# Kernel optimization log

Measured on AMD Instinct MI355X. Metric: run time of the kernel, lower is better.

## Reference

```python
import jax, jax.numpy as jnp
import numpy as np

D = 1024
H = 16
HD = D // H
EPS = 1e-5
NEG = -1e20


def _layernorm(x, w, b):
    m = jnp.mean(x, axis=-1, keepdims=True)
    v = jnp.mean((x - m) ** 2, axis=-1, keepdims=True)
    return (x - m) * jax.lax.rsqrt(v + EPS) * w + b


def setup_inputs() -> dict:
    key = jax.random.key(0)
    ks = jax.random.split(key, 16)
    s = 0.02
    inp = {
        "X": jax.random.normal(ks[0], (2, 2048, D), jnp.float32),
        "Wq": jax.random.normal(ks[1], (D, D), jnp.float32) * s,
        "bq": jnp.zeros((D,), jnp.float32),
        "Wk": jax.random.normal(ks[2], (D, D), jnp.float32) * s,
        "bk": jnp.zeros((D,), jnp.float32),
        "Wv": jax.random.normal(ks[3], (D, D), jnp.float32) * s,
        "bv": jnp.zeros((D,), jnp.float32),
        "Wo": jax.random.normal(ks[4], (D, D), jnp.float32) * s,
        "bo": jnp.zeros((D,), jnp.float32),
        "ln1_w": jnp.ones((D,), jnp.float32),
        "ln1_b": jnp.zeros((D,), jnp.float32),
        "Wup": jax.random.normal(ks[5], (4 * D, D), jnp.float32) * s,
        "bup": jnp.zeros((4 * D,), jnp.float32),
        "Wdown": jax.random.normal(ks[6], (D, 4 * D), jnp.float32) * s,
        "bdown": jnp.zeros((D,), jnp.float32),
        "ln2_w": jnp.ones((D,), jnp.float32),
        "ln2_b": jnp.zeros((D,), jnp.float32),
    }
    return inp


def reference(X, Wq, bq, Wk, bk, Wv, bv, Wo, bo, ln1_w, ln1_b,
              Wup, bup, Wdown, bdown, ln2_w, ln2_b):
    B, S, _ = X.shape
    # QKV projections -> [B, H, S, HD]
    q = (X @ Wq.T + bq).reshape(B, S, H, HD).transpose(0, 2, 1, 3)
    k = (X @ Wk.T + bk).reshape(B, S, H, HD).transpose(0, 2, 1, 3)
    v = (X @ Wv.T + bv).reshape(B, S, H, HD).transpose(0, 2, 1, 3)
    scores = jnp.einsum("bhqd,bhkd->bhqk", q, k) / jnp.sqrt(jnp.float32(HD))
    causal = jnp.tril(jnp.ones((S, S), dtype=bool))  # mask==0 -> -1e20
    scores = jnp.where(causal, scores, jnp.float32(NEG))
    attn = jax.nn.softmax(scores, axis=-1)  # dropout is identity in eval
    out = jnp.einsum("bhqk,bhkd->bhqd", attn, v)
    out = out.transpose(0, 2, 1, 3).reshape(B, S, D)
    out = out @ Wo.T + bo
    x = _layernorm(X + out, ln1_w, ln1_b)  # post-LN attention block
    up = jax.nn.relu(x @ Wup.T + bup)
    down = up @ Wdown.T + bdown
    return _layernorm(x + down, ln2_w, ln2_b)
```

## Files before the change

### kernel.cpp

```cpp
#include <hip/hip_runtime.h>
#include <stdint.h>

#define DMODEL 1024
#define NHEAD 16
#define HDIM 64
#define SEQ 2048
#define NBATCH 2
#define MTOK 4096

typedef float f32x4 __attribute__((ext_vector_type(4)));
typedef short s16x8 __attribute__((ext_vector_type(8)));
typedef unsigned short u16;
typedef u16 u16x4 __attribute__((ext_vector_type(4)));

typedef __attribute__((address_space(1))) const void* as1_cvp;
typedef __attribute__((address_space(3))) void* as3_vp;

__device__ inline u16 f2bf(float f) {
  uint32_t u = __float_as_uint(f);
  u = u + 0x7FFFu + ((u >> 16) & 1u);
  return (u16)(u >> 16);
}

__device__ inline uint32_t pk_bf16(float lo, float hi) {
  uint32_t r;
  asm("v_cvt_pk_bf16_f32 %0, %1, %2" : "=v"(r) : "v"(lo), "v"(hi));
  return r;
}

__device__ inline void gload_lds16(const void* g, void* l) {
  __builtin_amdgcn_global_load_lds((as1_cvp)g, (as3_vp)l, 16, 0, 0);
}

__global__ __launch_bounds__(256) void k_f2bf(const float* __restrict__ src,
                                              u16* __restrict__ dst, int n4) {
  int i = blockIdx.x * 256 + threadIdx.x;
  int stride = gridDim.x * 256;
  for (; i < n4; i += stride) {
    f32x4 v = ((const f32x4*)src)[i];
    u16x4 o;
    o[0] = f2bf(v[0]); o[1] = f2bf(v[1]); o[2] = f2bf(v[2]); o[3] = f2bf(v[3]);
    ((u16x4*)dst)[i] = o;
  }
}

__global__ __launch_bounds__(256) void k_f2bf_w4(
    const float* __restrict__ s0, const float* __restrict__ s1,
    const float* __restrict__ s2, const float* __restrict__ s3,
    u16* __restrict__ d0, u16* __restrict__ d1, u16* __restrict__ d2,
    u16* __restrict__ d3, int n4) {
  const float* src = blockIdx.y == 0 ? s0 : blockIdx.y == 1 ? s1
                     : blockIdx.y == 2 ? s2 : s3;
  u16* dst = blockIdx.y == 0 ? d0 : blockIdx.y == 1 ? d1
             : blockIdx.y == 2 ? d2 : d3;
  int i = blockIdx.x * 256 + threadIdx.x;
  int stride = gridDim.x * 256;
  for (; i < n4; i += stride) {
    f32x4 v = ((const f32x4*)src)[i];
    u16x4 o;
    o[0] = f2bf(v[0]); o[1] = f2bf(v[1]); o[2] = f2bf(v[2]); o[3] = f2bf(v[3]);
    ((u16x4*)dst)[i] = o;
  }
}

template <int MODE, int KSPL, int MH>
__global__ __launch_bounds__(512, 2) void k_gemm256(
    const u16* __restrict__ A, const u16* __restrict__ B,
    const float* __restrict__ bias, void* __restrict__ Cv,
    void* __restrict__ Cv1, int M, int N, int K) {
  constexpr int HALVES = MH + 2;
  __shared__ alignas(16) u16 lds[2 * HALVES * 8192];
  const int t = threadIdx.x;
  const int w = t >> 6;
  const int l = t & 63;
  const int wr = w >> 2;
  const int wc = w & 3;
  const int lr = l & 15, lg = l >> 4;
  const int r7 = lr & 7;
  const int lrow8 = l >> 3;

  const int gx = gridDim.x;
  int lin = blockIdx.y * gx + blockIdx.x;
  const int nwg = gx * gridDim.y;
  lin = (lin & 7) * (nwg >> 3) + (lin >> 3);
  const int bx = lin % gx, by = lin / gx;
  const int kz = KSPL > 1 ? blockIdx.z : 0;
  const int Kc = K / KSPL, kbeg = kz * Kc;
  const int brow = by * (MH * 128), bcol = bx * 256;

  constexpr int MF = MH * 4;
  const f32x4 Z4 = {0.f, 0.f, 0.f, 0.f};
  f32x4 acc[MF][4];
#pragma unroll
  for (int m = 0; m < MF; m++)
#pragma unroll
    for (int n = 0; n < 4; n++) acc[m][n] = Z4;

  const u16* Ag = A + (size_t)brow * K + kbeg;
  const u16* Bg = B + (size_t)bcol * K + kbeg;
  const int swz_src = ((l & 7) ^ ((l >> 3) & 7)) << 3;

  auto ldsH = [&](int buf, int half) { return lds + (buf * HALVES + half) * 8192; };
  auto stageA = [&](int kt, int buf) {
#pragma unroll
    for (int h = 0; h < MH; h++) {
      u16* lb = ldsH(buf, h);
      const int rb = h * 128;
      gload_lds16(Ag + (size_t)(rb + w * 8 + lrow8) * K + kt * 64 + swz_src,
                  lb + w * 512);
      gload_lds16(Ag + (size_t)(rb + 64 + w * 8 + lrow8) * K + kt * 64 + swz_src,
                  lb + (8 + w) * 512);
    }
  };
  auto stageB = [&](int kt, int buf) {
#pragma unroll
    for (int h = 0; h < 2; h++) {
      u16* lb = ldsH(buf, MH + h);
      const int rb = h * 128;
      gload_lds16(Bg + (size_t)(rb + w * 8 + lrow8) * K + kt * 64 + swz_src,
                  lb + w * 512);
      gload_lds16(Bg + (size_t)(rb + 64 + w * 8 + lrow8) * K + kt * 64 + swz_src,
                  lb + (8 + w) * 512);
    }
  };

  stageA(0, 0);
  stageB(0, 0);

  const int nkt = Kc >> 6;
  const int arb = (MH == 2) ? 0 : wr * 64;
  const int brb = (wc & 1) * 64;
  for (int kt = 0; kt < nkt; ++kt) {
    const int cur = kt & 1, nx = cur ^ 1;
    if (kt + 1 < nkt) {
      stageA(kt + 1, nx);
      if (MH == 2)
        asm volatile("s_waitcnt vmcnt(4)" ::: "memory");
      else
        asm volatile("s_waitcnt vmcnt(2)" ::: "memory");
    } else {
      asm volatile("s_waitcnt vmcnt(0)" ::: "memory");
    }
    __builtin_amdgcn_s_barrier();
    __builtin_amdgcn_sched_barrier(0);
    const u16* Ah = ldsH(cur, (MH == 2) ? wr : 0);
    const u16* Bh = ldsH(cur, MH + (wc >> 1));
#pragma unroll
    for (int kk = 0; kk < 2; kk++) {
      s16x8 bfr[4];
#pragma unroll
      for (int nf = 0; nf < 4; nf++)
        bfr[nf] = *(const s16x8*)(Bh + (brb + nf * 16 + lr) * 64 +
                                  (((kk * 4 + lg) ^ r7) << 3));
#pragma unroll
      for (int mh = 0; mh < MH; mh++) {
        s16x8 afr[4];
#pragma unroll
        for (int i = 0; i < 4; i++)
          afr[i] = *(const s16x8*)(Ah + (arb + (mh * 4 + i) * 16 + lr) * 64 +
                                   (((kk * 4 + lg) ^ r7) << 3));
        __builtin_amdgcn_s_setprio(1);
#pragma unroll
        for (int i = 0; i < 4; i++)
#pragma unroll
          for (int nf = 0; nf < 4; nf++)
            acc[mh * 4 + i][nf] = __builtin_amdgcn_mfma_f32_16x16x32_bf16(
                afr[i], bfr[nf], acc[mh * 4 + i][nf], 0, 0, 0);
        __builtin_amdgcn_s_setprio(0);
      }
      if (kk == 0 && kt + 1 < nkt) stageB(kt + 1, nx);
    }
    __builtin_amdgcn_sched_barrier(0);
    __builtin_amdgcn_s_barrier();
  }

  const int lg4 = lg * 4;
  const int wrb = wr * (MH == 2 ? 128 : 64);
  if (MODE == 0) {
    float* Co = (kz == 0) ? (float*)Cv : (float*)Cv1;
#pragma unroll
    for (int nf = 0; nf < 4; nf++) {
      const int col = bcol + wc * 64 + nf * 16 + lr;
      const float bvv = (kz == 0) ? bias[col] : 0.0f;
#pragma unroll
      for (int mf = 0; mf < MF; mf++) {
        const int row0 = brow + wrb + mf * 16 + lg4;
#pragma unroll
        for (int r = 0; r < 4; r++)
          Co[(size_t)(row0 + r) * N + col] = acc[mf][nf][r] + bvv;
      }
    }
  } else {
    u16* Sgw = lds + w * 2176;
    float bn[4];
#pragma unroll
    for (int nf = 0; nf < 4; nf++) bn[nf] = bias[bcol + wc * 64 + nf * 16 + lr];
    const int ch = l & 7;
#pragma unroll
    for (int hh = 0; hh < MH * 2; hh++) {
#pragma unroll
      for (int mm = 0; mm < 2; mm++) {
        const int mf = hh * 2 + mm;
#pragma unroll
        for (int nf = 0; nf < 4; nf++)
#pragma unroll
          for (int r = 0; r < 4; r++) {
            float vv = acc[mf][nf][r] + bn[nf];
            if (MODE == 2) vv = vv > 0.f ? vv : 0.f;
            Sgw[(mm * 16 + lg4 + r) * 68 + nf * 16 + lr] = f2bf(vv);
          }
      }
#pragma unroll
      for (int i = 0; i < 4; i++) {
        const int rr = i * 8 + (l >> 3);
        u16x4 a0 = *(const u16x4*)(Sgw + rr * 68 + ch * 8);
        u16x4 a1 = *(const u16x4*)(Sgw + rr * 68 + ch * 8 + 4);
        s16x8 v8;
#pragma unroll
        for (int j = 0; j < 4; j++) { v8[j] = (short)a0[j]; v8[4 + j] = (short)a1[j]; }
        *(s16x8*)((u16*)Cv + (size_t)(brow + wrb + hh * 32 + rr) * N +
                  (bcol + wc * 64 + ch * 8)) = v8;
      }
    }
  }
}

__global__ __launch_bounds__(512, 2) void k_gemm256_qkv(
    const u16* __restrict__ A, const u16* __restrict__ B,
    const float* __restrict__ bq, const float* __restrict__ bk,
    const float* __restrict__ bv, u16* __restrict__ qbf, u16* __restrict__ kbf,
    u16* __restrict__ vtbf, int M, int N, int K) {
  __shared__ alignas(16) u16 lds[2 * 4 * 8192];
  const int t = threadIdx.x;
  const int w = t >> 6, l = t & 63;
  const int wr = w >> 2, wc = w & 3;
  const int lr = l & 15, lg = l >> 4;
  const int r7 = lr & 7;
  const int lrow8 = l >> 3;

  const int gx = gridDim.x;
  int lin = blockIdx.y * gx + blockIdx.x;
  const int nwg = gx * gridDim.y;
  lin = (lin & 7) * (nwg >> 3) + (lin >> 3);
  const int bx = lin % gx, by = lin / gx;
  const int brow = by * 256, bcol = bx * 256;

  const f32x4 Z4 = {0.f, 0.f, 0.f, 0.f};
  f32x4 acc[8][4];
#pragma unroll
  for (int m = 0; m < 8; m++)
#pragma unroll
    for (int n = 0; n < 4; n++) acc[m][n] = Z4;

  const u16* Ag = A + (size_t)brow * K;
  const u16* Bg = B + (size_t)bcol * K;
  const int swz_src = ((l & 7) ^ ((l >> 3) & 7)) << 3;

  auto ldsH = [&](int buf, int half) { return lds + (buf * 4 + half) * 8192; };
  auto stageA = [&](int kt, int buf) {
#pragma unroll
    for (int h = 0; h < 2; h++) {
      u16* lb = ldsH(buf, h);
      const int rb = h * 128;
      gload_lds16(Ag + (size_t)(rb + w * 8 + lrow8) * K + kt * 64 + swz_src,
                  lb + w * 512);
      gload_lds16(Ag + (size_t)(rb + 64 + w * 8 + lrow8) * K + kt * 64 + swz_src,
                  lb + (8 + w) * 512);
    }
  };
  auto stageB = [&](int kt, int buf) {
#pragma unroll
    for (int h = 0; h < 2; h++) {
      u16* lb = ldsH(buf, 2 + h);
      const int rb = h * 128;
      gload_lds16(Bg + (size_t)(rb + w * 8 + lrow8) * K + kt * 64 + swz_src,
                  lb + w * 512);
      gload_lds16(Bg + (size_t)(rb + 64 + w * 8 + lrow8) * K + kt * 64 + swz_src,
                  lb + (8 + w) * 512);
    }
  };

  stageA(0, 0);
  stageB(0, 0);

  const int nkt = K >> 6;
  const int brb = (wc & 1) * 64;
  for (int kt = 0; kt < nkt; ++kt) {
    const int cur = kt & 1, nx = cur ^ 1;
    if (kt + 1 < nkt) {
      stageA(kt + 1, nx);
      asm volatile("s_waitcnt vmcnt(4)" ::: "memory");
    } else {
      asm volatile("s_waitcnt vmcnt(0)" ::: "memory");
    }
    __builtin_amdgcn_s_barrier();
    __builtin_amdgcn_sched_barrier(0);
    const u16* Ah = ldsH(cur, wr);
    const u16* Bh = ldsH(cur, 2 + (wc >> 1));
#pragma unroll
    for (int kk = 0; kk < 2; kk++) {
      s16x8 bfr[4];
#pragma unroll
      for (int nf = 0; nf < 4; nf++)
        bfr[nf] = *(const s16x8*)(Bh + (brb + nf * 16 + lr) * 64 +
                                  (((kk * 4 + lg) ^ r7) << 3));
#pragma unroll
      for (int mh = 0; mh < 2; mh++) {
        s16x8 afr[4];
#pragma unroll
        for (int i = 0; i < 4; i++)
          afr[i] = *(const s16x8*)(Ah + ((mh * 4 + i) * 16 + lr) * 64 +
                                   (((kk * 4 + lg) ^ r7) << 3));
        __builtin_amdgcn_s_setprio(1);
#pragma unroll
        for (int i = 0; i < 4; i++)
#pragma unroll
          for (int nf = 0; nf < 4; nf++)
            acc[mh * 4 + i][nf] = __builtin_amdgcn_mfma_f32_16x16x32_bf16(
                afr[i], bfr[nf], acc[mh * 4 + i][nf], 0, 0, 0);
        __builtin_amdgcn_s_setprio(0);
      }
      if (kk == 0 && kt + 1 < nkt) stageB(kt + 1, nx);
    }
    __builtin_amdgcn_sched_barrier(0);
    __builtin_amdgcn_s_barrier();
  }

  const int lg4 = lg * 4;
  const int wrb = wr * 128;
  u16* Sgw = lds + w * 2176;
  const int colw = bcol + wc * 64;
  const int region = colw >> 10;
  const int ck0 = colw & 1023;
  float bn[4];
  {
    const float* bb = region == 0 ? bq : region == 1 ? bk : bv;
#pragma unroll
    for (int nf = 0; nf < 4; nf++) bn[nf] = bb[ck0 + nf * 16 + lr];
  }
  const int ch = l & 7;
  if (region <= 1) {
#pragma unroll
    for (int hh = 0; hh < 4; hh++) {
#pragma unroll
      for (int mm = 0; mm < 2; mm++) {
        const int mf = hh * 2 + mm;
#pragma unroll
        for (int nf = 0; nf < 4; nf++)
#pragma unroll
          for (int r = 0; r < 4; r++) {
            float vv = acc[mf][nf][r] + bn[nf];
            if (region == 0) vv *= 0.125f;
            Sgw[(mm * 16 + lg4 + r) * 68 + nf * 16 + lr] = f2bf(vv);
          }
      }
#pragma unroll
      for (int i = 0; i < 4; i++) {
        const int rr = i * 8 + (l >> 3);
        u16x4 a0 = *(const u16x4*)(Sgw + rr * 68 + ch * 8);
        u16x4 a1 = *(const u16x4*)(Sgw + rr * 68 + ch * 8 + 4);
        s16x8 v8;
#pragma unroll
        for (int j = 0; j < 4; j++) { v8[j] = (short)a0[j]; v8[4 + j] = (short)a1[j]; }
        const int tok = brow + wrb + hh * 32 + rr;
        if (region == 0)
          *(s16x8*)(qbf + (size_t)tok * 1024 + ck0 + ch * 8) = v8;
        else
          *(s16x8*)(kbf + (size_t)tok * 1024 + ck0 + (((ch ^ tok) & 7) << 3)) =
              v8;
      }
    }
  } else {
    const int hcol = ck0 >> 6;
#pragma unroll
    for (int dh = 0; dh < 2; dh++)
#pragma unroll
      for (int th = 0; th < 2; th++) {
#pragma unroll
        for (int nn = 0; nn < 2; nn++) {
          const int nf = dh * 2 + nn;
#pragma unroll
          for (int mi = 0; mi < 4; mi++) {
            const int mf = th * 4 + mi;
#pragma unroll
            for (int r = 0; r < 4; r++)
              Sgw[(nn * 16 + lr) * 68 + mi * 16 + lg4 + r] =
                  f2bf(acc[mf][nf][r] + bn[nf]);
          }
        }
#pragma unroll
        for (int i = 0; i < 4; i++) {
          const int rr = i * 8 + (l >> 3);
          u16x4 a0 = *(const u16x4*)(Sgw + rr * 68 + ch * 8);
          u16x4 a1 = *(const u16x4*)(Sgw + rr * 68 + ch * 8 + 4);
          s16x8 v8;
#pragma unroll
          for (int j = 0; j < 4; j++) { v8[j] = (short)a0[j]; v8[4 + j] = (short)a1[j]; }
          const int d = dh * 32 + rr;
          const int tokb = brow + wrb + th * 64 + ch * 8;
          const int b = tokb >> 11, s64b = tokb & 2047;
          const int ssb = (s64b & ~63) + ((((s64b >> 3) ^ d) & 7) << 3);
          *(s16x8*)(vtbf + ((size_t)((b << 4) + hcol) * 64 + d) * 2048 + ssb) =
              v8;
        }
      }
  }
}

__global__ __launch_bounds__(256, 2) void k_attn(const u16* __restrict__ q,
                                                 const u16* __restrict__ kk,
                                                 const u16* __restrict__ vt,
                                                 u16* __restrict__ o) {
  __shared__ alignas(16) u16 Ks[2][64 * 64];
  __shared__ alignas(16) u16 Vs[2][64 * 64];
  __shared__ alignas(16) u16 Ps[4 * 16 * 64];
  const int t = threadIdx.x;
  const int w = t >> 6;
  const int l = t & 63;
  const int idx = blockIdx.x;
  const int bh = idx & 31;
  const int p = idx >> 5;
  const int b = bh >> 4, h = bh & 15;
  const u16* qb = q + (size_t)b * SEQ * DMODEL + h * HDIM;
  const u16* kb = kk + (size_t)b * SEQ * DMODEL + h * HDIM;
  const u16* vb = vt + (size_t)((b * 16 + h) * 64) * SEQ;

  const int sr = t >> 3;
  const int sc = (t & 7) * 8;
  const int lr = l & 15, lg = l >> 4;
  const int key = lr & 7;
  const f32x4 Z4 = {0.f, 0.f, 0.f, 0.f};
  u16* PsW = Ps + w * 1024;

  for (int half = 0; half < 2; half++) {
    const int qt = half ? (31 - p) : p;
    gload_lds16(qb + (size_t)(qt * 64 + sr) * DMODEL + sc, Ps + w * 512);
    gload_lds16(qb + (size_t)(qt * 64 + sr + 32) * DMODEL + sc,
                Ps + 2048 + w * 512);
    gload_lds16(kb + (size_t)sr * DMODEL + sc, &Ks[0][0] + w * 512);
    gload_lds16(kb + (size_t)(sr + 32) * DMODEL + sc,
                &Ks[0][0] + 2048 + w * 512);
    gload_lds16(vb + (size_t)sr * SEQ + sc, &Vs[0][0] + w * 512);
    gload_lds16(vb + (size_t)(sr + 32) * SEQ + sc, &Vs[0][0] + 2048 + w * 512);

    float m_l = -3.0e38f, l_l = 0.f;
    f32x4 oacc[4];
    for (int m = 0; m < 4; m++) oacc[m] = Z4;
    s16x8 bq0, bq1;

    for (int jt = 0; jt <= qt; jt++) {
      const int cur = jt & 1;
      if (jt < qt) {
        const int nx = cur ^ 1;
        gload_lds16(kb + (size_t)((jt + 1) * 64 + sr) * DMODEL + sc,
                    &Ks[nx][0] + w * 512);
        gload_lds16(kb + (size_t)((jt + 1) * 64 + sr + 32) * DMODEL + sc,
                    &Ks[nx][0] + 2048 + w * 512);
        gload_lds16(vb + (size_t)sr * SEQ + (jt + 1) * 64 + sc,
                    &Vs[nx][0] + w * 512);
        gload_lds16(vb + (size_t)(sr + 32) * SEQ + (jt + 1) * 64 + sc,
                    &Vs[nx][0] + 2048 + w * 512);
        asm volatile("s_waitcnt vmcnt(4)" ::: "memory");
      } else {
        asm volatile("s_waitcnt vmcnt(0)" ::: "memory");
      }
      __builtin_amdgcn_s_barrier();
      __builtin_amdgcn_sched_barrier(0);
      const u16* Kc = &Ks[cur][0];
      const u16* Vc = &Vs[cur][0];
      if (jt == 0) {
        bq0 = *(const s16x8*)(Ps + (w * 16 + lr) * 64 + lg * 8);
        bq1 = *(const s16x8*)(Ps + (w * 16 + lr) * 64 + 32 + lg * 8);
      }
      f32x4 sacc[4];
      for (int m = 0; m < 4; m++) sacc[m] = Z4;
      for (int m = 0; m < 4; m++) {
        s16x8 ak0 =
            *(const s16x8*)(Kc + (m * 16 + lr) * 64 + ((lg ^ key) << 3));
        s16x8 ak1 =
            *(const s16x8*)(Kc + (m * 16 + lr) * 64 + (((4 | lg) ^ key) << 3));
        sacc[m] = __builtin_amdgcn_mfma_f32_16x16x32_bf16(ak0, bq0, sacc[m], 0, 0, 0);
        sacc[m] = __builtin_amdgcn_mfma_f32_16x16x32_bf16(ak1, bq1, sacc[m], 0, 0, 0);
      }
      if (jt == qt) {
        const int q_rel = w * 16 + lr;
        for (int m = 0; m < 4; m++)
          for (int r = 0; r < 4; r++)
            if (m * 16 + lg * 4 + r > q_rel) sacc[m][r] = -3.0e38f;
      }
      float mx[4];
      for (int m = 0; m < 4; m++)
        mx[m] = fmaxf(fmaxf(sacc[m][0], sacc[m][1]),
                      fmaxf(sacc[m][2], sacc[m][3]));
      float pmax = fmaxf(fmaxf(mx[0], mx[1]), fmaxf(mx[2], mx[3]));
      pmax = fmaxf(pmax, __shfl_xor(pmax, 16, 64));
      pmax = fmaxf(pmax, __shfl_xor(pmax, 32, 64));
      if (!__all(pmax - m_l <= 8.0f)) {
        const float m_new = fmaxf(m_l, pmax);
        const float alpha = __expf(m_l - m_new);
        m_l = m_new;
        l_l *= alpha;
        for (int m = 0; m < 4; m++)
          for (int r = 0; r < 4; r++) oacc[m][r] *= alpha;
      }
      float p_[4][4], sm[4];
      for (int m = 0; m < 4; m++) {
        for (int r = 0; r < 4; r++) p_[m][r] = __expf(sacc[m][r] - m_l);
        sm[m] = (p_[m][0] + p_[m][1]) + (p_[m][2] + p_[m][3]);
      }
      float rs = (sm[0] + sm[1]) + (sm[2] + sm[3]);
      rs += __shfl_xor(rs, 16, 64);
      rs += __shfl_xor(rs, 32, 64);
      l_l += rs;
      for (int m = 0; m < 4; m++)
        for (int pr = 0; pr < 2; pr++) {
          const uint32_t pk = pk_bf16(p_[m][2 * pr], p_[m][2 * pr + 1]);
          const int kv0 = m * 16 + lg * 4 + 2 * pr;
          ((uint32_t*)PsW)[lr * 32 + (((kv0 >> 3) ^ key) << 2) +
                           ((kv0 >> 1) & 3)] = pk;
        }
      __builtin_amdgcn_sched_barrier(0);
      s16x8 bp0 = *(const s16x8*)(PsW + lr * 64 + ((lg ^ key) << 3));
      s16x8 bp1 = *(const s16x8*)(PsW + lr * 64 + (((4 | lg) ^ key) << 3));
      for (int m = 0; m < 4; m++) {
        s16x8 av0 =
            *(const s16x8*)(Vc + (m * 16 + lr) * 64 + ((lg ^ key) << 3));
        s16x8 av1 =
            *(const s16x8*)(Vc + (m * 16 + lr) * 64 + (((4 | lg) ^ key) << 3));
        oacc[m] = __builtin_amdgcn_mfma_f32_16x16x32_bf16(av0, bp0, oacc[m], 0, 0, 0);
        oacc[m] = __builtin_amdgcn_mfma_f32_16x16x32_bf16(av1, bp1, oacc[m], 0, 0, 0);
      }
      __builtin_amdgcn_sched_barrier(0);
      __builtin_amdgcn_s_barrier();
    }
    const float rl = 1.0f / l_l;
    const int tok = qt * 64 + w * 16 + lr;
    u16* orow = o + (size_t)(b * SEQ + tok) * DMODEL + h * HDIM;
    for (int m = 0; m < 4; m++)
      for (int pr = 0; pr < 2; pr++) {
        const uint32_t pk =
            pk_bf16(oacc[m][2 * pr] * rl, oacc[m][2 * pr + 1] * rl);
        *(uint32_t*)(orow + m * 16 + lg * 4 + 2 * pr) = pk;
      }
  }
}

__global__ __launch_bounds__(256) void k_add_ln(const float* __restrict__ X,
                                                const float* __restrict__ Y,
                                                const float* __restrict__ Y1,
                                                const float* __restrict__ w,
                                                const float* __restrict__ bias,
                                                float* __restrict__ of32,
                                                u16* __restrict__ obf) {
  __shared__ float sred[4];
  const int t = threadIdx.x;
  const size_t row = blockIdx.x;
  f32x4 xv = ((const f32x4*)(X + row * DMODEL))[t];
  f32x4 yv = ((const f32x4*)(Y + row * DMODEL))[t];
  f32x4 vv;
  for (int i = 0; i < 4; i++) vv[i] = xv[i] + yv[i];
  if (Y1) {
    f32x4 y1 = ((const f32x4*)(Y1 + row * DMODEL))[t];
    for (int i = 0; i < 4; i++) vv[i] += y1[i];
  }
  float s = vv[0] + vv[1] + vv[2] + vv[3];
  for (int off = 32; off >= 1; off >>= 1) s += __shfl_xor(s, off, 64);
  if ((t & 63) == 0) sred[t >> 6] = s;
  __syncthreads();
  s = sred[0] + sred[1] + sred[2] + sred[3];
  const float mean = s * (1.0f / DMODEL);
  f32x4 dv;
  for (int i = 0; i < 4; i++) dv[i] = vv[i] - mean;
  float ss = dv[0] * dv[0] + dv[1] * dv[1] + dv[2] * dv[2] + dv[3] * dv[3];
  __syncthreads();
  for (int off = 32; off >= 1; off >>= 1) ss += __shfl_xor(ss, off, 64);
  if ((t & 63) == 0) sred[t >> 6] = ss;
  __syncthreads();
  ss = sred[0] + sred[1] + sred[2] + sred[3];
  const float rs = rsqrtf(ss * (1.0f / DMODEL) + 1e-5f);
  f32x4 wv = ((const f32x4*)w)[t];
  f32x4 bv = ((const f32x4*)bias)[t];
  f32x4 ov;
  for (int i = 0; i < 4; i++) ov[i] = dv[i] * rs * wv[i] + bv[i];
  if (of32) ((f32x4*)(of32 + row * DMODEL))[t] = ov;
  if (obf) {
    u16x4 ob;
    for (int i = 0; i < 4; i++) ob[i] = f2bf(ov[i]);
    ((u16x4*)(obf + row * DMODEL))[t] = ob;
  }
}

extern "C" void kernel_launch(void* const* d_in, const int* in_sizes, int n_in,
                              void* d_out, int out_size, void* d_ws,
                              size_t ws_size, hipStream_t stream) {
  const float* X = (const float*)d_in[0];
  const float* Wq = (const float*)d_in[1];
  const float* bq = (const float*)d_in[2];
  const float* Wk = (const float*)d_in[3];
  const float* bk = (const float*)d_in[4];
  const float* Wv = (const float*)d_in[5];
  const float* bvp = (const float*)d_in[6];
  const float* Wo = (const float*)d_in[7];
  const float* bo = (const float*)d_in[8];
  const float* ln1w = (const float*)d_in[9];
  const float* ln1b = (const float*)d_in[10];
  const float* Wup = (const float*)d_in[11];
  const float* bup = (const float*)d_in[12];
  const float* Wdown = (const float*)d_in[13];
  const float* bdown = (const float*)d_in[14];
  const float* ln2w = (const float*)d_in[15];
  const float* ln2b = (const float*)d_in[16];

  char* ws = (char*)d_ws;
  const size_t MB = 1024 * 1024;
  u16* Xbf = (u16*)(ws + 0);
  u16* qbf = (u16*)(ws + 8 * MB);
  u16* kbf = (u16*)(ws + 16 * MB);
  u16* vtbf = (u16*)(ws + 24 * MB);
  u16* wqkv = (u16*)(ws + 32 * MB);
  u16* wo = (u16*)(ws + 38 * MB);
  u16* attnb = (u16*)(ws + 40 * MB);
  float* Ybuf = (float*)(ws + 48 * MB);
  float* xres = (float*)(ws + 64 * MB);
  u16* xbf = (u16*)(ws + 80 * MB);
  u16* upbf = (u16*)(ws + 0);
  u16* wbig = (u16*)(ws + 32 * MB);
  float* Ypart = (float*)d_out;

  const dim3 blk(256);
  k_f2bf<<<2048, blk, 0, stream>>>(X, Xbf, (MTOK * DMODEL) / 4);
  k_f2bf_w4<<<dim3(512, 4), blk, 0, stream>>>(
      Wq, Wk, Wv, Wo, wqkv + 0 * 1024 * 1024, wqkv + 1 * 1024 * 1024,
      wqkv + 2 * 1024 * 1024, wo, (DMODEL * DMODEL) / 4);

  k_gemm256_qkv<<<dim3(12, 16), dim3(512), 0, stream>>>(
      Xbf, wqkv, bq, bk, bvp, qbf, kbf, vtbf, MTOK, 3 * DMODEL, DMODEL);
  k_attn<<<16 * NBATCH * NHEAD, blk, 0, stream>>>(qbf, kbf, vtbf, attnb);
  k_gemm256<0, 2, 1><<<dim3(4, 32, 2), dim3(512), 0, stream>>>(
      attnb, wo, bo, Ybuf, Ypart, MTOK, DMODEL, DMODEL);
  k_add_ln<<<MTOK, blk, 0, stream>>>(X, Ybuf, Ypart, ln1w, ln1b, xres, xbf);

  k_f2bf<<<2048, blk, 0, stream>>>(Wup, wbig, (4 * DMODEL * DMODEL) / 4);
  k_gemm256<2, 1, 2><<<dim3(16, 16), dim3(512), 0, stream>>>(
      xbf, wbig, bup, upbf, nullptr, MTOK, 4 * DMODEL, DMODEL);
  k_f2bf<<<2048, blk, 0, stream>>>(Wdown, wbig, (4 * DMODEL * DMODEL) / 4);
  k_gemm256<0, 2, 1><<<dim3(4, 32, 2), dim3(512), 0, stream>>>(
      upbf, wbig, bdown, Ybuf, Ypart, MTOK, DMODEL, 4 * DMODEL);
  k_add_ln<<<MTOK, blk, 0, stream>>>(xres, Ybuf, Ypart, ln2w, ln2b,
                                     (float*)d_out, (u16*)nullptr);
}
```

Before: 211.2 us.

## Process paired causal query tiles in one shared K/V pass

The attention kernel used to handle its two query tiles (p and 31-p) one after the other, loading K/V tiles twice. It now walks the K/V sequence once and computes both query tiles at the same time, so each loaded K/V tile feeds both. The short tile only participates while jt <= p. The block-to-p mapping is also reordered so blocks with larger work are scheduled first. The cost is more registers (two accumulator sets) and double the P staging space in LDS, which may lower occupancy.

```diff
diff --git a/kernel.cpp b/kernel.cpp
--- a/kernel.cpp
+++ b/kernel.cpp
@@ -413,13 +413,16 @@
                                                  u16* __restrict__ o) {
   __shared__ alignas(16) u16 Ks[2][64 * 64];
   __shared__ alignas(16) u16 Vs[2][64 * 64];
-  __shared__ alignas(16) u16 Ps[4 * 16 * 64];
+  __shared__ alignas(16) u16 Ps[2][4 * 16 * 64];
   const int t = threadIdx.x;
   const int w = t >> 6;
   const int l = t & 63;
   const int idx = blockIdx.x;
   const int bh = idx & 31;
-  const int p = idx >> 5;
+  const int pp = idx >> 5;
+  const int p = (pp < 8) ? pp : (23 - pp);
+  const int qtA = p, qtB = 31 - p;
+  const int nt = 32 - p;
   const int b = bh >> 4, h = bh & 15;
   const u16* qb = q + (size_t)b * SEQ * DMODEL + h * HDIM;
   const u16* kb = kk + (size_t)b * SEQ * DMODEL + h * HDIM;
@@ -430,116 +433,184 @@
   const int lr = l & 15, lg = l >> 4;
   const int key = lr & 7;
   const f32x4 Z4 = {0.f, 0.f, 0.f, 0.f};
-  u16* PsW = Ps + w * 1024;
-
-  for (int half = 0; half < 2; half++) {
-    const int qt = half ? (31 - p) : p;
-    gload_lds16(qb + (size_t)(qt * 64 + sr) * DMODEL + sc, Ps + w * 512);
-    gload_lds16(qb + (size_t)(qt * 64 + sr + 32) * DMODEL + sc,
-                Ps + 2048 + w * 512);
-    gload_lds16(kb + (size_t)sr * DMODEL + sc, &Ks[0][0] + w * 512);
-    gload_lds16(kb + (size_t)(sr + 32) * DMODEL + sc,
-                &Ks[0][0] + 2048 + w * 512);
-    gload_lds16(vb + (size_t)sr * SEQ + sc, &Vs[0][0] + w * 512);
-    gload_lds16(vb + (size_t)(sr + 32) * SEQ + sc, &Vs[0][0] + 2048 + w * 512);
-
-    float m_l = -3.0e38f, l_l = 0.f;
-    f32x4 oacc[4];
-    for (int m = 0; m < 4; m++) oacc[m] = Z4;
-    s16x8 bq0, bq1;
-
-    for (int jt = 0; jt <= qt; jt++) {
-      const int cur = jt & 1;
-      if (jt < qt) {
-        const int nx = cur ^ 1;
-        gload_lds16(kb + (size_t)((jt + 1) * 64 + sr) * DMODEL + sc,
-                    &Ks[nx][0] + w * 512);
-        gload_lds16(kb + (size_t)((jt + 1) * 64 + sr + 32) * DMODEL + sc,
-                    &Ks[nx][0] + 2048 + w * 512);
-        gload_lds16(vb + (size_t)sr * SEQ + (jt + 1) * 64 + sc,
-                    &Vs[nx][0] + w * 512);
-        gload_lds16(vb + (size_t)(sr + 32) * SEQ + (jt + 1) * 64 + sc,
-                    &Vs[nx][0] + 2048 + w * 512);
-        asm volatile("s_waitcnt vmcnt(4)" ::: "memory");
-      } else {
-        asm volatile("s_waitcnt vmcnt(0)" ::: "memory");
-      }
-      __builtin_amdgcn_s_barrier();
-      __builtin_amdgcn_sched_barrier(0);
-      const u16* Kc = &Ks[cur][0];
-      const u16* Vc = &Vs[cur][0];
-      if (jt == 0) {
-        bq0 = *(const s16x8*)(Ps + (w * 16 + lr) * 64 + lg * 8);
-        bq1 = *(const s16x8*)(Ps + (w * 16 + lr) * 64 + 32 + lg * 8);
-      }
-      f32x4 sacc[4];
-      for (int m = 0; m < 4; m++) sacc[m] = Z4;
-      for (int m = 0; m < 4; m++) {
-        s16x8 ak0 =
-            *(const s16x8*)(Kc + (m * 16 + lr) * 64 + ((lg ^ key) << 3));
-        s16x8 ak1 =
-            *(const s16x8*)(Kc + (m * 16 + lr) * 64 + (((4 | lg) ^ key) << 3));
-        sacc[m] = __builtin_amdgcn_mfma_f32_16x16x32_bf16(ak0, bq0, sacc[m], 0, 0, 0);
-        sacc[m] = __builtin_amdgcn_mfma_f32_16x16x32_bf16(ak1, bq1, sacc[m], 0, 0, 0);
-      }
-      if (jt == qt) {
-        const int q_rel = w * 16 + lr;
-        for (int m = 0; m < 4; m++)
-          for (int r = 0; r < 4; r++)
-            if (m * 16 + lg * 4 + r > q_rel) sacc[m][r] = -3.0e38f;
-      }
+  u16* PsA = &Ps[0][0] + w * 1024;
+  u16* PsB = &Ps[1][0] + w * 1024;
+
+  gload_lds16(qb + (size_t)(qtA * 64 + sr) * DMODEL + sc, &Ps[0][0] + w * 512);
+  gload_lds16(qb + (size_t)(qtA * 64 + sr + 32) * DMODEL + sc,
+              &Ps[0][0] + 2048 + w * 512);
+  gload_lds16(qb + (size_t)(qtB * 64 + sr) * DMODEL + sc, &Ps[1][0] + w * 512);
+  gload_lds16(qb + (size_t)(qtB * 64 + sr + 32) * DMODEL + sc,
+              &Ps[1][0] + 2048 + w * 512);
+  gload_lds16(kb + (size_t)sr * DMODEL + sc, &Ks[0][0] + w * 512);
+  gload_lds16(kb + (size_t)(sr + 32) * DMODEL + sc, &Ks[0][0] + 2048 + w * 512);
+  gload_lds16(vb + (size_t)sr * SEQ + sc, &Vs[0][0] + w * 512);
+  gload_lds16(vb + (size_t)(sr + 32) * SEQ + sc, &Vs[0][0] + 2048 + w * 512);
+
+  float m_lA = -3.0e38f, l_lA = 0.f, m_lB = -3.0e38f, l_lB = 0.f;
+  f32x4 oaccA[4], oaccB[4];
+  for (int m = 0; m < 4; m++) { oaccA[m] = Z4; oaccB[m] = Z4; }
+  s16x8 bqA0, bqA1, bqB0, bqB1;
+
+  for (int jt = 0; jt < nt; jt++) {
+    const int cur = jt & 1;
+    if (jt + 1 < nt) {
+      const int nx = cur ^ 1;
+      gload_lds16(kb + (size_t)((jt + 1) * 64 + sr) * DMODEL + sc,
+                  &Ks[nx][0] + w * 512);
+      gload_lds16(kb + (size_t)((jt + 1) * 64 + sr + 32) * DMODEL + sc,
+                  &Ks[nx][0] + 2048 + w * 512);
+      gload_lds16(vb + (size_t)sr * SEQ + (jt + 1) * 64 + sc,
+                  &Vs[nx][0] + w * 512);
+      gload_lds16(vb + (size_t)(sr + 32) * SEQ + (jt + 1) * 64 + sc,
+                  &Vs[nx][0] + 2048 + w * 512);
+      asm volatile("s_waitcnt vmcnt(4)" ::: "memory");
+    } else {
+      asm volatile("s_waitcnt vmcnt(0)" ::: "memory");
+    }
+    __builtin_amdgcn_s_barrier();
+    __builtin_amdgcn_sched_barrier(0);
+    const u16* Kc = &Ks[cur][0];
+    const u16* Vc = &Vs[cur][0];
+    if (jt == 0) {
+      bqA0 = *(const s16x8*)(&Ps[0][0] + (w * 16 + lr) * 64 + lg * 8);
+      bqA1 = *(const s16x8*)(&Ps[0][0] + (w * 16 + lr) * 64 + 32 + lg * 8);
+      bqB0 = *(const s16x8*)(&Ps[1][0] + (w * 16 + lr) * 64 + lg * 8);
+      bqB1 = *(const s16x8*)(&Ps[1][0] + (w * 16 + lr) * 64 + 32 + lg * 8);
+    }
+    const bool aact = (jt <= p);
+    f32x4 saccA[4], saccB[4];
+    for (int m = 0; m < 4; m++) { saccA[m] = Z4; saccB[m] = Z4; }
+    for (int m = 0; m < 4; m++) {
+      s16x8 ak0 = *(const s16x8*)(Kc + (m * 16 + lr) * 64 + ((lg ^ key) << 3));
+      s16x8 ak1 =
+          *(const s16x8*)(Kc + (m * 16 + lr) * 64 + (((4 | lg) ^ key) << 3));
+      saccB[m] = __builtin_amdgcn_mfma_f32_16x16x32_bf16(ak0, bqB0, saccB[m], 0, 0, 0);
+      saccB[m] = __builtin_amdgcn_mfma_f32_16x16x32_bf16(ak1, bqB1, saccB[m], 0, 0, 0);
+      if (aact) {
+        saccA[m] = __builtin_amdgcn_mfma_f32_16x16x32_bf16(ak0, bqA0, saccA[m], 0, 0, 0);
+        saccA[m] = __builtin_amdgcn_mfma_f32_16x16x32_bf16(ak1, bqA1, saccA[m], 0, 0, 0);
+      }
+    }
+    if (jt == nt - 1) {
+      const int q_rel = w * 16 + lr;
+      for (int m = 0; m < 4; m++)
+        for (int r = 0; r < 4; r++)
+          if (m * 16 + lg * 4 + r > q_rel) saccB[m][r] = -3.0e38f;
+    }
+    if (aact && jt == p) {
+      const int q_rel = w * 16 + lr;
+      for (int m = 0; m < 4; m++)
+        for (int r = 0; r < 4; r++)
+          if (m * 16 + lg * 4 + r > q_rel) saccA[m][r] = -3.0e38f;
+    }
+    {
       float mx[4];
       for (int m = 0; m < 4; m++)
-        mx[m] = fmaxf(fmaxf(sacc[m][0], sacc[m][1]),
-                      fmaxf(sacc[m][2], sacc[m][3]));
+        mx[m] = fmaxf(fmaxf(saccB[m][0], saccB[m][1]),
+                      fmaxf(saccB[m][2], saccB[m][3]));
       float pmax = fmaxf(fmaxf(mx[0], mx[1]), fmaxf(mx[2], mx[3]));
       pmax = fmaxf(pmax, __shfl_xor(pmax, 16, 64));
       pmax = fmaxf(pmax, __shfl_xor(pmax, 32, 64));
-      if (!__all(pmax - m_l <= 8.0f)) {
-        const float m_new = fmaxf(m_l, pmax);
-        const float alpha = __expf(m_l - m_new);
-        m_l = m_new;
-        l_l *= alpha;
+      if (!__all(pmax - m_lB <= 8.0f)) {
+        const float m_new = fmaxf(m_lB, pmax);
+        const float alpha = __expf(m_lB - m_new);
+        m_lB = m_new;
+        l_lB *= alpha;
         for (int m = 0; m < 4; m++)
-          for (int r = 0; r < 4; r++) oacc[m][r] *= alpha;
+          for (int r = 0; r < 4; r++) oaccB[m][r] *= alpha;
       }
       float p_[4][4], sm[4];
       for (int m = 0; m < 4; m++) {
-        for (int r = 0; r < 4; r++) p_[m][r] = __expf(sacc[m][r] - m_l);
+        for (int r = 0; r < 4; r++) p_[m][r] = __expf(saccB[m][r] - m_lB);
         sm[m] = (p_[m][0] + p_[m][1]) + (p_[m][2] + p_[m][3]);
       }
       float rs = (sm[0] + sm[1]) + (sm[2] + sm[3]);
       rs += __shfl_xor(rs, 16, 64);
       rs += __shfl_xor(rs, 32, 64);
-      l_l += rs;
+      l_lB += rs;
       for (int m = 0; m < 4; m++)
         for (int pr = 0; pr < 2; pr++) {
           const uint32_t pk = pk_bf16(p_[m][2 * pr], p_[m][2 * pr + 1]);
           const int kv0 = m * 16 + lg * 4 + 2 * pr;
-          ((uint32_t*)PsW)[lr * 32 + (((kv0 >> 3) ^ key) << 2) +
+          ((uint32_t*)PsB)[lr * 32 + (((kv0 >> 3) ^ key) << 2) +
                            ((kv0 >> 1) & 3)] = pk;
         }
-      __builtin_amdgcn_sched_barrier(0);
-      s16x8 bp0 = *(const s16x8*)(PsW + lr * 64 + ((lg ^ key) << 3));
-      s16x8 bp1 = *(const s16x8*)(PsW + lr * 64 + (((4 | lg) ^ key) << 3));
+    }
+    if (aact) {
+      float mx[4];
+      for (int m = 0; m < 4; m++)
+        mx[m] = fmaxf(fmaxf(saccA[m][0], saccA[m][1]),
+                      fmaxf(saccA[m][2], saccA[m][3]));
+      float pmax = fmaxf(fmaxf(mx[0], mx[1]), fmaxf(mx[2], mx[3]));
+      pmax = fmaxf(pmax, __shfl_xor(pmax, 16, 64));
+      pmax = fmaxf(pmax, __shfl_xor(pmax, 32, 64));
+      if (!__all(pmax - m_lA <= 8.0f)) {
+        const float m_new = fmaxf(m_lA, pmax);
+        const float alpha = __expf(m_lA - m_new);
+        m_lA = m_new;
+        l_lA *= alpha;
+        for (int m = 0; m < 4; m++)
+          for (int r = 0; r < 4; r++) oaccA[m][r] *= alpha;
+      }
+      float p_[4][4], sm[4];
       for (int m = 0; m < 4; m++) {
-        s16x8 av0 =
-            *(const s16x8*)(Vc + (m * 16 + lr) * 64 + ((lg ^ key) << 3));
-        s16x8 av1 =
-            *(const s16x8*)(Vc + (m * 16 + lr) * 64 + (((4 | lg) ^ key) << 3));
-        oacc[m] = __builtin_amdgcn_mfma_f32_16x16x32_bf16(av0, bp0, oacc[m], 0, 0, 0);
-        oacc[m] = __builtin_amdgcn_mfma_f32_16x16x32_bf16(av1, bp1, oacc[m], 0, 0, 0);
-      }
-      __builtin_amdgcn_sched_barrier(0);
-      __builtin_amdgcn_s_barrier();
-    }
-    const float rl = 1.0f / l_l;
-    const int tok = qt * 64 + w * 16 + lr;
+        for (int r = 0; r < 4; r++) p_[m][r] = __expf(saccA[m][r] - m_lA);
+        sm[m] = (p_[m][0] + p_[m][1]) + (p_[m][2] + p_[m][3]);
+      }
+      float rs = (sm[0] + sm[1]) + (sm[2] + sm[3]);
+      rs += __shfl_xor(rs, 16, 64);
+      rs += __shfl_xor(rs, 32, 64);
+      l_lA += rs;
+      for (int m = 0; m < 4; m++)
+        for (int pr = 0; pr < 2; pr++) {
+          const uint32_t pk = pk_bf16(p_[m][2 * pr], p_[m][2 * pr + 1]);
+          const int kv0 = m * 16 + lg * 4 + 2 * pr;
+          ((uint32_t*)PsA)[lr * 32 + (((kv0 >> 3) ^ key) << 2) +
+                           ((kv0 >> 1) & 3)] = pk;
+        }
+    }
+    __builtin_amdgcn_sched_barrier(0);
+    s16x8 bpB0 = *(const s16x8*)(PsB + lr * 64 + ((lg ^ key) << 3));
+    s16x8 bpB1 = *(const s16x8*)(PsB + lr * 64 + (((4 | lg) ^ key) << 3));
+    s16x8 bpA0, bpA1;
+    if (aact) {
+      bpA0 = *(const s16x8*)(PsA + lr * 64 + ((lg ^ key) << 3));
+      bpA1 = *(const s16x8*)(PsA + lr * 64 + (((4 | lg) ^ key) << 3));
+    }
+    for (int m = 0; m < 4; m++) {
+      s16x8 av0 = *(const s16x8*)(Vc + (m * 16 + lr) * 64 + ((lg ^ key) << 3));
+      s16x8 av1 =
+          *(const s16x8*)(Vc + (m * 16 + lr) * 64 + (((4 | lg) ^ key) << 3));
+      oaccB[m] = __builtin_amdgcn_mfma_f32_16x16x32_bf16(av0, bpB0, oaccB[m], 0, 0, 0);
+      oaccB[m] = __builtin_amdgcn_mfma_f32_16x16x32_bf16(av1, bpB1, oaccB[m], 0, 0, 0);
+      if (aact) {
+        oaccA[m] = __builtin_amdgcn_mfma_f32_16x16x32_bf16(av0, bpA0, oaccA[m], 0, 0, 0);
+        oaccA[m] = __builtin_amdgcn_mfma_f32_16x16x32_bf16(av1, bpA1, oaccA[m], 0, 0, 0);
+      }
+    }
+    __builtin_amdgcn_sched_barrier(0);
+    __builtin_amdgcn_s_barrier();
+  }
+  {
+    const float rl = 1.0f / l_lA;
+    const int tok = qtA * 64 + w * 16 + lr;
     u16* orow = o + (size_t)(b * SEQ + tok) * DMODEL + h * HDIM;
     for (int m = 0; m < 4; m++)
       for (int pr = 0; pr < 2; pr++) {
         const uint32_t pk =
-            pk_bf16(oacc[m][2 * pr] * rl, oacc[m][2 * pr + 1] * rl);
+            pk_bf16(oaccA[m][2 * pr] * rl, oaccA[m][2 * pr + 1] * rl);
+        *(uint32_t*)(orow + m * 16 + lg * 4 + 2 * pr) = pk;
+      }
+  }
+  {
+    const float rl = 1.0f / l_lB;
+    const int tok = qtB * 64 + w * 16 + lr;
+    u16* orow = o + (size_t)(b * SEQ + tok) * DMODEL + h * HDIM;
+    for (int m = 0; m < 4; m++)
+      for (int pr = 0; pr < 2; pr++) {
+        const uint32_t pk =
+            pk_bf16(oaccB[m][2 * pr] * rl, oaccB[m][2 * pr + 1] * rl);
         *(uint32_t*)(orow + m * 16 + lg * 4 + 2 * pr) = pk;
       }
   }
```

After: 214.3 us. No clear change (+1.5%).

## Process 128-key KV tiles per iteration in causal attention kernel

Applied to the files above, without the earlier changes.

Doubles the key/value tile per loop iteration from 64 to 128 keys, split into two 64-key sub-buffers, so each iteration issues twice the MFMA work per barrier and softmax rescale check. Q is now staged into each wave's private P buffer instead of a shared region. This reduces loop overhead and synchronisation count. In exchange it doubles shared memory use, adds register pressure from 8 score accumulators, and wastes some masked compute on the diagonal tile.

```diff
diff --git a/kernel.cpp b/kernel.cpp
--- a/kernel.cpp
+++ b/kernel.cpp
@@ -411,9 +411,9 @@
                                                  const u16* __restrict__ kk,
                                                  const u16* __restrict__ vt,
                                                  u16* __restrict__ o) {
-  __shared__ alignas(16) u16 Ks[2][64 * 64];
-  __shared__ alignas(16) u16 Vs[2][64 * 64];
-  __shared__ alignas(16) u16 Ps[4 * 16 * 64];
+  __shared__ alignas(16) u16 Ks[2][2][64 * 64];
+  __shared__ alignas(16) u16 Vs[2][2][64 * 64];
+  __shared__ alignas(16) u16 Ps[4][2][16 * 64];
   const int t = threadIdx.x;
   const int w = t >> 6;
   const int l = t & 63;
@@ -430,69 +430,87 @@
   const int lr = l & 15, lg = l >> 4;
   const int key = lr & 7;
   const f32x4 Z4 = {0.f, 0.f, 0.f, 0.f};
-  u16* PsW = Ps + w * 1024;
+  u16* PsBase = &Ps[0][0][0];
+  u16* PsW = PsBase + w * 2048;
 
   for (int half = 0; half < 2; half++) {
     const int qt = half ? (31 - p) : p;
-    gload_lds16(qb + (size_t)(qt * 64 + sr) * DMODEL + sc, Ps + w * 512);
-    gload_lds16(qb + (size_t)(qt * 64 + sr + 32) * DMODEL + sc,
-                Ps + 2048 + w * 512);
-    gload_lds16(kb + (size_t)sr * DMODEL + sc, &Ks[0][0] + w * 512);
-    gload_lds16(kb + (size_t)(sr + 32) * DMODEL + sc,
-                &Ks[0][0] + 2048 + w * 512);
-    gload_lds16(vb + (size_t)sr * SEQ + sc, &Vs[0][0] + w * 512);
-    gload_lds16(vb + (size_t)(sr + 32) * SEQ + sc, &Vs[0][0] + 2048 + w * 512);
+    const int nt = (qt >> 1) + 1;
+    gload_lds16(qb + (size_t)(qt * 64 + w * 16 + (l >> 3)) * DMODEL + (l & 7) * 8,
+                PsW);
+    gload_lds16(
+        qb + (size_t)(qt * 64 + w * 16 + 8 + (l >> 3)) * DMODEL + (l & 7) * 8,
+        PsW + 512);
+#pragma unroll
+    for (int s = 0; s < 2; s++) {
+      gload_lds16(kb + (size_t)(s * 64 + sr) * DMODEL + sc,
+                  &Ks[0][s][0] + w * 512);
+      gload_lds16(kb + (size_t)(s * 64 + sr + 32) * DMODEL + sc,
+                  &Ks[0][s][0] + 2048 + w * 512);
+      gload_lds16(vb + (size_t)sr * SEQ + s * 64 + sc, &Vs[0][s][0] + w * 512);
+      gload_lds16(vb + (size_t)(sr + 32) * SEQ + s * 64 + sc,
+                  &Vs[0][s][0] + 2048 + w * 512);
+    }
 
     float m_l = -3.0e38f, l_l = 0.f;
     f32x4 oacc[4];
+#pragma unroll
     for (int m = 0; m < 4; m++) oacc[m] = Z4;
     s16x8 bq0, bq1;
 
-    for (int jt = 0; jt <= qt; jt++) {
+    for (int jt = 0; jt < nt; jt++) {
       const int cur = jt & 1;
-      if (jt < qt) {
+      if (jt + 1 < nt) {
         const int nx = cur ^ 1;
-        gload_lds16(kb + (size_t)((jt + 1) * 64 + sr) * DMODEL + sc,
-                    &Ks[nx][0] + w * 512);
-        gload_lds16(kb + (size_t)((jt + 1) * 64 + sr + 32) * DMODEL + sc,
-                    &Ks[nx][0] + 2048 + w * 512);
-        gload_lds16(vb + (size_t)sr * SEQ + (jt + 1) * 64 + sc,
-                    &Vs[nx][0] + w * 512);
-        gload_lds16(vb + (size_t)(sr + 32) * SEQ + (jt + 1) * 64 + sc,
-                    &Vs[nx][0] + 2048 + w * 512);
-        asm volatile("s_waitcnt vmcnt(4)" ::: "memory");
+        const int kvb = (jt + 1) * 128;
+#pragma unroll
+        for (int s = 0; s < 2; s++) {
+          gload_lds16(kb + (size_t)(kvb + s * 64 + sr) * DMODEL + sc,
+                      &Ks[nx][s][0] + w * 512);
+          gload_lds16(kb + (size_t)(kvb + s * 64 + sr + 32) * DMODEL + sc,
+                      &Ks[nx][s][0] + 2048 + w * 512);
+          gload_lds16(vb + (size_t)sr * SEQ + kvb + s * 64 + sc,
+                      &Vs[nx][s][0] + w * 512);
+          gload_lds16(vb + (size_t)(sr + 32) * SEQ + kvb + s * 64 + sc,
+                      &Vs[nx][s][0] + 2048 + w * 512);
+        }
+        asm volatile("s_waitcnt vmcnt(8)" ::: "memory");
       } else {
         asm volatile("s_waitcnt vmcnt(0)" ::: "memory");
       }
       __builtin_amdgcn_s_barrier();
       __builtin_amdgcn_sched_barrier(0);
-      const u16* Kc = &Ks[cur][0];
-      const u16* Vc = &Vs[cur][0];
       if (jt == 0) {
-        bq0 = *(const s16x8*)(Ps + (w * 16 + lr) * 64 + lg * 8);
-        bq1 = *(const s16x8*)(Ps + (w * 16 + lr) * 64 + 32 + lg * 8);
-      }
-      f32x4 sacc[4];
-      for (int m = 0; m < 4; m++) sacc[m] = Z4;
-      for (int m = 0; m < 4; m++) {
-        s16x8 ak0 =
-            *(const s16x8*)(Kc + (m * 16 + lr) * 64 + ((lg ^ key) << 3));
-        s16x8 ak1 =
-            *(const s16x8*)(Kc + (m * 16 + lr) * 64 + (((4 | lg) ^ key) << 3));
+        bq0 = *(const s16x8*)(PsW + lr * 64 + lg * 8);
+        bq1 = *(const s16x8*)(PsW + lr * 64 + 32 + lg * 8);
+      }
+      f32x4 sacc[8];
+#pragma unroll
+      for (int m = 0; m < 8; m++) sacc[m] = Z4;
+#pragma unroll
+      for (int m = 0; m < 8; m++) {
+        const u16* Kc = &Ks[cur][m >> 2][0];
+        const int rr = (m & 3) * 16 + lr;
+        s16x8 ak0 = *(const s16x8*)(Kc + rr * 64 + ((lg ^ key) << 3));
+        s16x8 ak1 = *(const s16x8*)(Kc + rr * 64 + (((4 | lg) ^ key) << 3));
         sacc[m] = __builtin_amdgcn_mfma_f32_16x16x32_bf16(ak0, bq0, sacc[m], 0, 0, 0);
         sacc[m] = __builtin_amdgcn_mfma_f32_16x16x32_bf16(ak1, bq1, sacc[m], 0, 0, 0);
       }
-      if (jt == qt) {
-        const int q_rel = w * 16 + lr;
-        for (int m = 0; m < 4; m++)
+      if (jt == nt - 1) {
+        const int qg = qt * 64 + w * 16 + lr - jt * 128;
+#pragma unroll
+        for (int m = 0; m < 8; m++)
+#pragma unroll
           for (int r = 0; r < 4; r++)
-            if (m * 16 + lg * 4 + r > q_rel) sacc[m][r] = -3.0e38f;
-      }
-      float mx[4];
-      for (int m = 0; m < 4; m++)
+            if (m * 16 + lg * 4 + r > qg) sacc[m][r] = -3.0e38f;
+      }
+      float mx[8];
+#pragma unroll
+      for (int m = 0; m < 8; m++)
         mx[m] = fmaxf(fmaxf(sacc[m][0], sacc[m][1]),
                       fmaxf(sacc[m][2], sacc[m][3]));
-      float pmax = fmaxf(fmaxf(mx[0], mx[1]), fmaxf(mx[2], mx[3]));
+      float pmax = fmaxf(fmaxf(fmaxf(mx[0], mx[1]), fmaxf(mx[2], mx[3])),
+                         fmaxf(fmaxf(mx[4], mx[5]), fmaxf(mx[6], mx[7])));
       pmax = fmaxf(pmax, __shfl_xor(pmax, 16, 64));
       pmax = fmaxf(pmax, __shfl_xor(pmax, 32, 64));
       if (!__all(pmax - m_l <= 8.0f)) {
@@ -500,35 +518,45 @@
         const float alpha = __expf(m_l - m_new);
         m_l = m_new;
         l_l *= alpha;
+#pragma unroll
         for (int m = 0; m < 4; m++)
+#pragma unroll
           for (int r = 0; r < 4; r++) oacc[m][r] *= alpha;
       }
-      float p_[4][4], sm[4];
-      for (int m = 0; m < 4; m++) {
+      float p_[8][4], sm[8];
+#pragma unroll
+      for (int m = 0; m < 8; m++) {
+#pragma unroll
         for (int r = 0; r < 4; r++) p_[m][r] = __expf(sacc[m][r] - m_l);
         sm[m] = (p_[m][0] + p_[m][1]) + (p_[m][2] + p_[m][3]);
       }
-      float rs = (sm[0] + sm[1]) + (sm[2] + sm[3]);
+      float rs = ((sm[0] + sm[1]) + (sm[2] + sm[3])) +
+                 ((sm[4] + sm[5]) + (sm[6] + sm[7]));
       rs += __shfl_xor(rs, 16, 64);
       rs += __shfl_xor(rs, 32, 64);
       l_l += rs;
-      for (int m = 0; m < 4; m++)
+#pragma unroll
+      for (int m = 0; m < 8; m++)
+#pragma unroll
         for (int pr = 0; pr < 2; pr++) {
           const uint32_t pk = pk_bf16(p_[m][2 * pr], p_[m][2 * pr + 1]);
           const int kv0 = m * 16 + lg * 4 + 2 * pr;
-          ((uint32_t*)PsW)[lr * 32 + (((kv0 >> 3) ^ key) << 2) +
-                           ((kv0 >> 1) & 3)] = pk;
+          const int sub = kv0 >> 6, kvp = kv0 & 63;
+          ((uint32_t*)(PsW + sub * 1024))[lr * 32 + (((kvp >> 3) ^ key) << 2) +
+                                          ((kvp >> 1) & 3)] = pk;
         }
       __builtin_amdgcn_sched_barrier(0);
-      s16x8 bp0 = *(const s16x8*)(PsW + lr * 64 + ((lg ^ key) << 3));
-      s16x8 bp1 = *(const s16x8*)(PsW + lr * 64 + (((4 | lg) ^ key) << 3));
-      for (int m = 0; m < 4; m++) {
-        s16x8 av0 =
-            *(const s16x8*)(Vc + (m * 16 + lr) * 64 + ((lg ^ key) << 3));
-        s16x8 av1 =
-            *(const s16x8*)(Vc + (m * 16 + lr) * 64 + (((4 | lg) ^ key) << 3));
-        oacc[m] = __builtin_amdgcn_mfma_f32_16x16x32_bf16(av0, bp0, oacc[m], 0, 0, 0);
-        oacc[m] = __builtin_amdgcn_mfma_f32_16x16x32_bf16(av1, bp1, oacc[m], 0, 0, 0);
+#pragma unroll
+      for (int ks = 0; ks < 4; ks++) {
+        const int sub = ks >> 1;
+        const int c = (ks & 1) * 4 + lg;
+        s16x8 bp = *(const s16x8*)(PsW + sub * 1024 + lr * 64 + ((c ^ key) << 3));
+        const u16* Vc = &Vs[cur][sub][0];
+#pragma unroll
+        for (int m = 0; m < 4; m++) {
+          s16x8 av = *(const s16x8*)(Vc + (m * 16 + lr) * 64 + ((c ^ key) << 3));
+          oacc[m] = __builtin_amdgcn_mfma_f32_16x16x32_bf16(av, bp, oacc[m], 0, 0, 0);
+        }
       }
       __builtin_amdgcn_sched_barrier(0);
       __builtin_amdgcn_s_barrier();
@@ -536,7 +564,9 @@
     const float rl = 1.0f / l_l;
     const int tok = qt * 64 + w * 16 + lr;
     u16* orow = o + (size_t)(b * SEQ + tok) * DMODEL + h * HDIM;
+#pragma unroll
     for (int m = 0; m < 4; m++)
+#pragma unroll
       for (int pr = 0; pr < 2; pr++) {
         const uint32_t pk =
             pk_bf16(oacc[m][2 * pr] * rl, oacc[m][2 * pr + 1] * rl);
```

Result: faster. 206.9 us (-2.1%).
